# Performance work log

Measured on AMD Instinct MI355X. Metric: run time of the kernel, lower is better.

Reference implementation:

```python
import jax, jax.numpy as jnp
import numpy as np
import math

D_MODEL = 1024
N_HEAD = 16
B, T = 4, 2048


def setup_inputs() -> dict:
    key = jax.random.key(0)
    ks = jax.random.split(key, 12)
    s = 1.0 / math.sqrt(D_MODEL)
    inp = {
        "q": jax.random.normal(ks[0], (B, T, D_MODEL), dtype=jnp.float32),
        "k": jax.random.normal(ks[1], (B, T, D_MODEL), dtype=jnp.float32),
        "v": jax.random.normal(ks[2], (B, T, D_MODEL), dtype=jnp.float32),
        "Wq": jax.random.uniform(ks[3], (D_MODEL, D_MODEL), jnp.float32, -s, s),
        "bq": jax.random.uniform(ks[4], (D_MODEL,), jnp.float32, -s, s),
        "Wk": jax.random.uniform(ks[5], (D_MODEL, D_MODEL), jnp.float32, -s, s),
        "bk": jax.random.uniform(ks[6], (D_MODEL,), jnp.float32, -s, s),
        "Wv": jax.random.uniform(ks[7], (D_MODEL, D_MODEL), jnp.float32, -s, s),
        "bv": jax.random.uniform(ks[8], (D_MODEL,), jnp.float32, -s, s),
        "Wo": jax.random.uniform(ks[9], (D_MODEL, D_MODEL), jnp.float32, -s, s),
        "bo": jax.random.uniform(ks[10], (D_MODEL,), jnp.float32, -s, s),
    }
    return inp


def reference(q, k, v, Wq, bq, Wk, bk, Wv, bv, Wo, bo):
    # NOTE: original module applies all three projections to `q` (k, v args unused)
    batch, time, dim = q.shape
    n_d = dim // N_HEAD
    # torch Linear: x @ W.T + b
    Q = (q @ Wq.T + bq).reshape(batch, time, N_HEAD, n_d).transpose(0, 2, 1, 3)
    K = (q @ Wk.T + bk).reshape(batch, time, N_HEAD, n_d).transpose(0, 2, 1, 3)
    V = (q @ Wv.T + bv).reshape(batch, time, N_HEAD, n_d).transpose(0, 2, 1, 3)
    # [B, H, T, T]
    score = jnp.einsum("bhqd,bhkd->bhqk", Q, K) / jnp.sqrt(jnp.float32(n_d))
    causal = jnp.tril(jnp.ones((time, time), dtype=bool))
    score = jnp.where(causal, score, -jnp.inf)
    # original uses Softmax(dim=-2): normalizes over the QUERY axis (faithful)
    attn = jax.nn.softmax(score, axis=-2)
    ctx = jnp.einsum("bhqk,bhkd->bhqd", attn, V)
    ctx = ctx.transpose(0, 2, 1, 3).reshape(batch, time, dim)
    return ctx @ Wo.T + bo
```

## Files before the change

kernel.cpp:

```cpp
#include <hip/hip_runtime.h>
#include <hip/hip_bf16.h>
#include <cstdint>
#include <cstddef>

typedef __bf16 bf16x8 __attribute__((ext_vector_type(8)));
typedef __bf16 bf16x4 __attribute__((ext_vector_type(4)));
typedef __bf16 bf16x2 __attribute__((ext_vector_type(2)));
typedef float  f32x4  __attribute__((ext_vector_type(4)));

static constexpr int TSEQ  = 2048;
static constexpr int DM    = 1024;
static constexpr int NH    = 16;
static constexpr int HD    = 64;
static constexpr int BATCH = 4;
static constexpr float SCL = 0.18033688011112042f;

__device__ __forceinline__ void gload16(const __bf16* g, __bf16* l) {
  __builtin_amdgcn_global_load_lds((const __attribute__((address_space(1))) void*)g,
                                   (__attribute__((address_space(3))) void*)l, 16, 0, 0);
}

#define PBAR()  asm volatile("s_barrier" ::: "memory")
#define LGKM0() do { asm volatile("s_waitcnt lgkmcnt(0)" ::: "memory"); \
                     __builtin_amdgcn_sched_barrier(0); } while (0)

__global__ __launch_bounds__(256) void cvt_kernel(const float* __restrict__ in,
                                                  __bf16* __restrict__ out, int n4) {
  int i = blockIdx.x * 256 + threadIdx.x;
  if (i < n4) {
    float4 v = reinterpret_cast<const float4*>(in)[i];
    bf16x4 o;
    o[0] = (__bf16)v.x; o[1] = (__bf16)v.y; o[2] = (__bf16)v.z; o[3] = (__bf16)v.w;
    reinterpret_cast<bf16x4*>(out)[i] = o;
  }
}

__global__ __launch_bounds__(256) void cvt4_kernel(
    const float* __restrict__ a, const float* __restrict__ bsrc,
    const float* __restrict__ c, const float* __restrict__ d,
    __bf16* __restrict__ oa, __bf16* __restrict__ ob,
    __bf16* __restrict__ oc, __bf16* __restrict__ od, int n4) {
  const float* src = (blockIdx.y == 0) ? a : (blockIdx.y == 1) ? bsrc
                    : (blockIdx.y == 2) ? c : d;
  __bf16* dst = (blockIdx.y == 0) ? oa : (blockIdx.y == 1) ? ob
               : (blockIdx.y == 2) ? oc : od;
  int i = blockIdx.x * 256 + threadIdx.x;
  if (i < n4) {
    float4 v = reinterpret_cast<const float4*>(src)[i];
    bf16x4 o;
    o[0] = (__bf16)v.x; o[1] = (__bf16)v.y; o[2] = (__bf16)v.z; o[3] = (__bf16)v.w;
    reinterpret_cast<bf16x4*>(dst)[i] = o;
  }
}

template <typename OUT_T>
__device__ __forceinline__ void gemm_body8(
    const __bf16* __restrict__ A, const __bf16* __restrict__ W,
    const float* __restrict__ bias, OUT_T* __restrict__ C,
    int i0, int o0, __bf16* lA, __bf16* lB) {
  const int tid = threadIdx.x;
  const int l = tid & 63, lr = l & 15, lg = l >> 4;
  const int w = tid >> 6;
  const int wr = w >> 2, wc = w & 3;

  f32x4 acc[8][4];
  const f32x4 fzero = {0.f, 0.f, 0.f, 0.f};
#pragma unroll
  for (int mi = 0; mi < 8; ++mi)
#pragma unroll
    for (int ni = 0; ni < 4; ++ni) acc[mi][ni] = fzero;

  const int s_row = tid >> 3;
  const int s_cc  = tid & 7;
  const __bf16* Ab = A + (size_t)i0 * DM;
  const __bf16* Wb = W + (size_t)o0 * DM;

  auto stage = [&](const __bf16* G, __bf16* L, int buf, int kt, int h) {
#pragma unroll
    for (int rr = 0; rr < 2; ++rr) {
      int row = h * 128 + rr * 64 + s_row;
      gload16(G + (size_t)row * DM + kt * 64 + ((s_cc ^ (row & 7)) << 3),
              L + buf * 16384 + (h * 128 + rr * 64) * 64 + tid * 8);
    }
  };
  auto rd = [&](const __bf16* base, int row, int ks) {
    int chunk = (ks * 4 + lg) ^ (row & 7);
    return *(const bf16x8*)(base + row * 64 + chunk * 8);
  };

  const int NT = DM / 64;

#pragma unroll
  for (int h = 0; h < 2; ++h) { stage(Ab, lA, 0, 0, h); stage(Wb, lB, 0, 0, h); }
#pragma unroll
  for (int h = 0; h < 2; ++h) { stage(Ab, lA, 1, 1, h); stage(Wb, lB, 1, 1, h); }
  asm volatile("s_waitcnt vmcnt(8)" ::: "memory");
  PBAR();

  for (int t = 0; t < NT; ++t) {
    const int cur = t & 1;
    const __bf16* cA = lA + cur * 16384;
    const __bf16* cB = lB + cur * 16384;
    const bool pre = (t + 2 < NT);

    bf16x8 afl[4][2], bfl[2][2], afh[4][2], bfh[2][2];

#pragma unroll
    for (int mi = 0; mi < 4; ++mi)
#pragma unroll
      for (int ks = 0; ks < 2; ++ks)
        afl[mi][ks] = rd(cA, wr * 64 + mi * 16 + lr, ks);
#pragma unroll
    for (int ni = 0; ni < 2; ++ni)
#pragma unroll
      for (int ks = 0; ks < 2; ++ks)
        bfl[ni][ks] = rd(cB, wc * 32 + ni * 16 + lr, ks);
    PBAR(); LGKM0();
    __builtin_amdgcn_s_setprio(1);
#pragma unroll
    for (int mi = 0; mi < 4; ++mi)
#pragma unroll
      for (int ni = 0; ni < 2; ++ni)
#pragma unroll
        for (int ks = 0; ks < 2; ++ks)
          acc[mi][ni] = __builtin_amdgcn_mfma_f32_16x16x32_bf16(
              afl[mi][ks], bfl[ni][ks], acc[mi][ni], 0, 0, 0);
    __builtin_amdgcn_s_setprio(0);
    PBAR();

#pragma unroll
    for (int ni = 0; ni < 2; ++ni)
#pragma unroll
      for (int ks = 0; ks < 2; ++ks)
        bfh[ni][ks] = rd(cB, 128 + wc * 32 + ni * 16 + lr, ks);
    if (pre) stage(Wb, lB, cur, t + 2, 0);
    PBAR(); LGKM0();
    __builtin_amdgcn_s_setprio(1);
#pragma unroll
    for (int mi = 0; mi < 4; ++mi)
#pragma unroll
      for (int ni = 0; ni < 2; ++ni)
#pragma unroll
        for (int ks = 0; ks < 2; ++ks)
          acc[mi][ni + 2] = __builtin_amdgcn_mfma_f32_16x16x32_bf16(
              afl[mi][ks], bfh[ni][ks], acc[mi][ni + 2], 0, 0, 0);
    __builtin_amdgcn_s_setprio(0);
    PBAR();

#pragma unroll
    for (int mi = 0; mi < 4; ++mi)
#pragma unroll
      for (int ks = 0; ks < 2; ++ks)
        afh[mi][ks] = rd(cA, 128 + wr * 64 + mi * 16 + lr, ks);
    if (pre) { stage(Ab, lA, cur, t + 2, 0); stage(Wb, lB, cur, t + 2, 1); }
    PBAR(); LGKM0();
    __builtin_amdgcn_s_setprio(1);
#pragma unroll
    for (int mi = 0; mi < 4; ++mi)
#pragma unroll
      for (int ni = 0; ni < 2; ++ni)
#pragma unroll
        for (int ks = 0; ks < 2; ++ks)
          acc[mi + 4][ni] = __builtin_amdgcn_mfma_f32_16x16x32_bf16(
              afh[mi][ks], bfl[ni][ks], acc[mi + 4][ni], 0, 0, 0);
    __builtin_amdgcn_s_setprio(0);
    PBAR();

    if (pre) stage(Ab, lA, cur, t + 2, 1);
    if (pre)                asm volatile("s_waitcnt vmcnt(8)" ::: "memory");
    else if (t + 1 < NT)    asm volatile("s_waitcnt vmcnt(0)" ::: "memory");
    PBAR();
    __builtin_amdgcn_s_setprio(1);
#pragma unroll
    for (int mi = 0; mi < 4; ++mi)
#pragma unroll
      for (int ni = 0; ni < 2; ++ni)
#pragma unroll
        for (int ks = 0; ks < 2; ++ks)
          acc[mi + 4][ni + 2] = __builtin_amdgcn_mfma_f32_16x16x32_bf16(
              afh[mi][ks], bfh[ni][ks], acc[mi + 4][ni + 2], 0, 0, 0);
    __builtin_amdgcn_s_setprio(0);
    PBAR();
  }

#pragma unroll
  for (int ni = 0; ni < 4; ++ni) {
    int colb = (ni < 2) ? (wc * 32 + ni * 16) : (128 + wc * 32 + (ni - 2) * 16);
    int col = o0 + colb + lr;
    float bb = bias[col];
#pragma unroll
    for (int mi = 0; mi < 8; ++mi) {
      int rowb = (mi < 4) ? (wr * 64 + mi * 16) : (128 + wr * 64 + (mi - 4) * 16);
      int row = i0 + rowb + lg * 4;
#pragma unroll
      for (int r = 0; r < 4; ++r)
        C[(size_t)(row + r) * DM + col] = (OUT_T)(acc[mi][ni][r] + bb);
    }
  }
}

__global__ __launch_bounds__(512, 2) void gemm_qkv_kernel(
    const __bf16* __restrict__ A,
    const __bf16* __restrict__ W0, const __bf16* __restrict__ W1,
    const __bf16* __restrict__ W2,
    const float* __restrict__ b0, const float* __restrict__ b1,
    const float* __restrict__ b2,
    __bf16* __restrict__ O0, __bf16* __restrict__ O1, __bf16* __restrict__ O2) {
  __shared__ __align__(16) __bf16 lA[2 * 256 * 64];
  __shared__ __align__(16) __bf16 lB[2 * 256 * 64];
  const int flat = blockIdx.x;
  const int xcd = flat & 7, idx = flat >> 3;
  const int mi = xcd * 4 + idx / 12;
  const int nig = idx % 12;
  const int z = nig >> 2;
  const int o0 = (nig & 3) * 256;
  const __bf16* W = (z == 0) ? W0 : (z == 1) ? W1 : W2;
  const float* bias = (z == 0) ? b0 : (z == 1) ? b1 : b2;
  __bf16* C = (z == 0) ? O0 : (z == 1) ? O1 : O2;
  gemm_body8<__bf16>(A, W, bias, C, mi * 256, o0, lA, lB);
}

template <typename OUT_T>
__device__ __forceinline__ void gemm_body2(
    const __bf16* __restrict__ A, const __bf16* __restrict__ W,
    const float* __restrict__ bias, OUT_T* __restrict__ C,
    int i0, int o0, __bf16* lA, __bf16* lB) {
  const int tid = threadIdx.x;
  const int l = tid & 63, lr = l & 15, lg = l >> 4;
  const int w = tid >> 6;
  const int wr = w >> 2, wc = w & 3;

  f32x4 acc[4][4];
  const f32x4 fzero = {0.f, 0.f, 0.f, 0.f};
#pragma unroll
  for (int mi = 0; mi < 4; ++mi)
#pragma unroll
    for (int ni = 0; ni < 4; ++ni) acc[mi][ni] = fzero;

  const int s_row = tid >> 3;
  const int s_cc  = tid & 7;
  const int NT = DM / 64;

  {
#pragma unroll
    for (int n = 0; n < 2; ++n) {
      int row = n * 64 + s_row;
      gload16(A + (size_t)(i0 + row) * DM + ((s_cc ^ (row & 7)) << 3),
              lA + n * 4096 + tid * 8);
    }
#pragma unroll
    for (int n = 0; n < 4; ++n) {
      int row = n * 64 + s_row;
      gload16(W + (size_t)(o0 + row) * DM + ((s_cc ^ (row & 7)) << 3),
              lB + n * 4096 + tid * 8);
    }
  }
  asm volatile("s_waitcnt vmcnt(0)" ::: "memory");
  __syncthreads();

  for (int t = 0; t < NT; ++t) {
    const int cur = t & 1;
    if (t + 1 < NT) {
      const int k0 = (t + 1) * 64;
      const int nxt = cur ^ 1;
#pragma unroll
      for (int n = 0; n < 2; ++n) {
        int row = n * 64 + s_row;
        gload16(A + (size_t)(i0 + row) * DM + k0 + ((s_cc ^ (row & 7)) << 3),
                lA + nxt * 8192 + n * 4096 + tid * 8);
      }
#pragma unroll
      for (int n = 0; n < 4; ++n) {
        int row = n * 64 + s_row;
        gload16(W + (size_t)(o0 + row) * DM + k0 + ((s_cc ^ (row & 7)) << 3),
                lB + nxt * 16384 + n * 4096 + tid * 8);
      }
    }

    const __bf16* cA = lA + cur * 8192;
    const __bf16* cB = lB + cur * 16384;

    bf16x8 af[4][2], bf_[2][2];
#pragma unroll
    for (int mi = 0; mi < 4; ++mi)
#pragma unroll
      for (int ks = 0; ks < 2; ++ks) {
        int row = wr * 64 + mi * 16 + lr;
        int chunk = (ks * 4 + lg) ^ (row & 7);
        af[mi][ks] = *(const bf16x8*)(cA + row * 64 + chunk * 8);
      }
#pragma unroll
    for (int ni = 0; ni < 2; ++ni)
#pragma unroll
      for (int ks = 0; ks < 2; ++ks) {
        int row = wc * 64 + ni * 16 + lr;
        int chunk = (ks * 4 + lg) ^ (row & 7);
        bf_[ni][ks] = *(const bf16x8*)(cB + row * 64 + chunk * 8);
      }
    __builtin_amdgcn_s_setprio(1);
#pragma unroll
    for (int mi = 0; mi < 4; ++mi)
#pragma unroll
      for (int ni = 0; ni < 2; ++ni)
#pragma unroll
        for (int ks = 0; ks < 2; ++ks)
          acc[mi][ni] = __builtin_amdgcn_mfma_f32_16x16x32_bf16(
              af[mi][ks], bf_[ni][ks], acc[mi][ni], 0, 0, 0);
    __builtin_amdgcn_s_setprio(0);

#pragma unroll
    for (int ni = 0; ni < 2; ++ni)
#pragma unroll
      for (int ks = 0; ks < 2; ++ks) {
        int row = wc * 64 + (ni + 2) * 16 + lr;
        int chunk = (ks * 4 + lg) ^ (row & 7);
        bf_[ni][ks] = *(const bf16x8*)(cB + row * 64 + chunk * 8);
      }
    __builtin_amdgcn_s_setprio(1);
#pragma unroll
    for (int mi = 0; mi < 4; ++mi)
#pragma unroll
      for (int ni = 0; ni < 2; ++ni)
#pragma unroll
        for (int ks = 0; ks < 2; ++ks)
          acc[mi][ni + 2] = __builtin_amdgcn_mfma_f32_16x16x32_bf16(
              af[mi][ks], bf_[ni][ks], acc[mi][ni + 2], 0, 0, 0);
    __builtin_amdgcn_s_setprio(0);

    if (t + 1 < NT) {
      asm volatile("s_waitcnt vmcnt(0)" ::: "memory");
      __syncthreads();
    }
  }

#pragma unroll
  for (int ni = 0; ni < 4; ++ni) {
    int col = o0 + wc * 64 + ni * 16 + lr;
    float bb = bias[col];
#pragma unroll
    for (int mi = 0; mi < 4; ++mi) {
      int row = i0 + wr * 64 + mi * 16 + lg * 4;
#pragma unroll
      for (int r = 0; r < 4; ++r)
        C[(size_t)(row + r) * DM + col] = (OUT_T)(acc[mi][ni][r] + bb);
    }
  }
}

__global__ __launch_bounds__(512, 2) void gemm_out_kernel(
    const __bf16* __restrict__ A, const __bf16* __restrict__ W,
    const float* __restrict__ bias, float* __restrict__ C) {
  __shared__ __align__(16) __bf16 lA[2 * 128 * 64];
  __shared__ __align__(16) __bf16 lB[2 * 256 * 64];
  const int flat = blockIdx.x;
  const int xcd = flat & 7, idx = flat >> 3;
  const int mi = xcd * 8 + (idx & 7);
  const int ni = idx >> 3;
  gemm_body2<float>(A, W, bias, C, mi * 128, ni * 256, lA, lB);
}

__global__ __launch_bounds__(256) void colstats_kernel(
    const __bf16* __restrict__ Q, const __bf16* __restrict__ K,
    const __bf16* __restrict__ V, __bf16* __restrict__ VT) {
  const int flat = blockIdx.x;
  const int wid = (flat & 7) * 128 + (flat >> 3);
  const int g = wid >> 4, bx = wid & 15;
  const int h = g & 15, b = g >> 4;
  const int tid = threadIdx.x;
  const int w = tid >> 6, l = tid & 63, lr = l & 15, lg = l >> 4;
  const size_t base = (size_t)b * TSEQ * DM + (size_t)h * HD;

  __shared__ float part[4][64];
  __shared__ float invc[64];

  for (int ph = 0; ph < 2; ++ph) {
    const int kt = ph ? (31 - bx) : bx;
    const int k0 = kt * 64;

    bf16x8 kf[4][2];
#pragma unroll
    for (int ct = 0; ct < 4; ++ct)
#pragma unroll
      for (int ks = 0; ks < 2; ++ks)
        kf[ct][ks] = *(const bf16x8*)(K + base + (size_t)(k0 + ct * 16 + lr) * DM +
                                      ks * 32 + lg * 8);

    float csum[4] = {0.f, 0.f, 0.f, 0.f};
    const int nchunks = (TSEQ - k0) >> 4;
    for (int jj = w; jj < nchunks; jj += 4) {
      int qrow = k0 + jj * 16;
      bf16x8 a0 = *(const bf16x8*)(Q + base + (size_t)(qrow + lr) * DM + lg * 8);
      bf16x8 a1 = *(const bf16x8*)(Q + base + (size_t)(qrow + lr) * DM + 32 + lg * 8);
      const bool interior = (jj >= 4);
#pragma unroll
      for (int ct = 0; ct < 4; ++ct) {
        f32x4 s = {0.f, 0.f, 0.f, 0.f};
        s = __builtin_amdgcn_mfma_f32_16x16x32_bf16(a0, kf[ct][0], s, 0, 0, 0);
        s = __builtin_amdgcn_mfma_f32_16x16x32_bf16(a1, kf[ct][1], s, 0, 0, 0);
        if (interior) {
#pragma unroll
          for (int r = 0; r < 4; ++r) csum[ct] += __builtin_amdgcn_exp2f(s[r] * SCL);
        } else {
#pragma unroll
          for (int r = 0; r < 4; ++r) {
            int ql = jj * 16 + lg * 4 + r;
            int kl = ct * 16 + lr;
            float e = __builtin_amdgcn_exp2f(s[r] * SCL);
            csum[ct] += (ql >= kl) ? e : 0.f;
          }
        }
      }
    }

#pragma unroll
    for (int ct = 0; ct < 4; ++ct) {
      csum[ct] += __shfl_xor(csum[ct], 16, 64);
      csum[ct] += __shfl_xor(csum[ct], 32, 64);
    }

    if (l < 16) {
#pragma unroll
      for (int ct = 0; ct < 4; ++ct) part[w][ct * 16 + l] = csum[ct];
    }
    __syncthreads();
    if (tid < 64) {
      float c = part[0][tid] + part[1][tid] + part[2][tid] + part[3][tid];
      invc[tid] = 1.0f / c;
    }
    __syncthreads();

    const int d = tid >> 2, gq = tid & 3;
    size_t vtb = (((size_t)(b * NH + h)) * HD + d) * TSEQ + k0 + gq * 16;
#pragma unroll
    for (int kc = 0; kc < 16; kc += 2) {
      int kl = gq * 16 + kc;
      float v0 = (float)V[base + (size_t)(k0 + kl) * DM + d] * invc[kl];
      float v1 = (float)V[base + (size_t)(k0 + kl + 1) * DM + d] * invc[kl + 1];
      bf16x2 o; o[0] = (__bf16)v0; o[1] = (__bf16)v1;
      *(bf16x2*)(VT + vtb + kc) = o;
    }
    __syncthreads();
  }
}

__device__ __forceinline__ int swz(int e) { return e ^ (((e >> 6) & 7) << 3); }

__global__ __launch_bounds__(256) void ctx_kernel(
    const __bf16* __restrict__ Q, const __bf16* __restrict__ K,
    const __bf16* __restrict__ VT, __bf16* __restrict__ CTX) {
  __shared__ __align__(16) __bf16 lK[4096];
  __shared__ __align__(16) __bf16 lV[4096];
  __shared__ __align__(16) __bf16 lP[4][16 * 88];
  const int flat = blockIdx.x;
  const int wid = (flat & 7) * 128 + (flat >> 3);
  const int g = wid >> 4, bx = wid & 15;
  const int h = g & 15, b = g >> 4;
  const int tid = threadIdx.x;
  const int w = tid >> 6, l = tid & 63, lr = l & 15, lg = l >> 4;
  const size_t base = (size_t)b * TSEQ * DM + (size_t)h * HD;
  const size_t vtb = ((size_t)(b * NH + h)) * HD * TSEQ;
  __bf16* pw = &lP[w][0];

  const int srow = w * 8 + (l >> 3);
  const int scol = (((l & 7) ^ (l >> 3)) << 3);

  for (int ph = 0; ph < 2; ++ph) {
    const int qt = ph ? bx : 31 - bx;
    const int q0 = qt * 64;

    bf16x8 qf[2];
#pragma unroll
    for (int ks = 0; ks < 2; ++ks)
      qf[ks] = *(const bf16x8*)(Q + base + (size_t)(q0 + w * 16 + lr) * DM + ks * 32 + lg * 8);

    f32x4 acc[4];
    const f32x4 fzero = {0.f, 0.f, 0.f, 0.f};
#pragma unroll
    for (int dt = 0; dt < 4; ++dt) acc[dt] = fzero;

    for (int kt = 0; kt <= qt; ++kt) {
      const int k0 = kt * 64;
#pragma unroll
      for (int n = 0; n < 2; ++n) {
        gload16(K + base + (size_t)(k0 + n * 32 + srow) * DM + scol,
                lK + n * 2048 + w * 512);
        gload16(VT + vtb + (size_t)(n * 32 + srow) * TSEQ + k0 + scol,
                lV + n * 2048 + w * 512);
      }
      asm volatile("s_waitcnt vmcnt(0)" ::: "memory");
      __syncthreads();

      const bool diag = (kt == qt);
#pragma unroll
      for (int ct = 0; ct < 4; ++ct) {
        f32x4 s = {0.f, 0.f, 0.f, 0.f};
#pragma unroll
        for (int ks = 0; ks < 2; ++ks) {
          int e = (ct * 16 + lr) * 64 + ks * 32 + lg * 8;
          bf16x8 kb8 = *(const bf16x8*)(lK + swz(e));
          s = __builtin_amdgcn_mfma_f32_16x16x32_bf16(kb8, qf[ks], s, 0, 0, 0);
        }
        bf16x4 pk;
        if (diag) {
#pragma unroll
          for (int r = 0; r < 4; ++r) {
            int ql = w * 16 + lr;
            int kl = ct * 16 + lg * 4 + r;
            float pv = (ql >= kl) ? __builtin_amdgcn_exp2f(s[r] * SCL) : 0.f;
            pk[r] = (__bf16)pv;
          }
        } else {
#pragma unroll
          for (int r = 0; r < 4; ++r)
            pk[r] = (__bf16)__builtin_amdgcn_exp2f(s[r] * SCL);
        }
        *(bf16x4*)(pw + lr * 88 + ct * 16 + lg * 4) = pk;
      }
      asm volatile("" ::: "memory");

      bf16x8 pa[2];
#pragma unroll
      for (int ks = 0; ks < 2; ++ks)
        pa[ks] = *(const bf16x8*)(pw + lr * 88 + ks * 32 + lg * 8);
#pragma unroll
      for (int dt = 0; dt < 4; ++dt) {
#pragma unroll
        for (int ks = 0; ks < 2; ++ks) {
          int e = (dt * 16 + lr) * 64 + ks * 32 + lg * 8;
          bf16x8 vb8 = *(const bf16x8*)(lV + swz(e));
          acc[dt] = __builtin_amdgcn_mfma_f32_16x16x32_bf16(pa[ks], vb8, acc[dt], 0, 0, 0);
        }
      }
      __syncthreads();
    }

#pragma unroll
    for (int dt = 0; dt < 4; ++dt)
#pragma unroll
      for (int r = 0; r < 4; ++r)
        CTX[base + (size_t)(q0 + w * 16 + lg * 4 + r) * DM + dt * 16 + lr] = (__bf16)acc[dt][r];
  }
}

extern "C" void kernel_launch(void* const* d_in, const int* in_sizes, int n_in,
                              void* d_out, int out_size, void* d_ws, size_t ws_size,
                              hipStream_t stream) {
  const float* q  = (const float*)d_in[0];
  const float* Wq = (const float*)d_in[3];
  const float* bq = (const float*)d_in[4];
  const float* Wk = (const float*)d_in[5];
  const float* bk = (const float*)d_in[6];
  const float* Wv = (const float*)d_in[7];
  const float* bv = (const float*)d_in[8];
  const float* Wo = (const float*)d_in[9];
  const float* bo = (const float*)d_in[10];
  float* out = (float*)d_out;

  const size_t NTOK = (size_t)BATCH * TSEQ;
  char* ws = (char*)d_ws;
  __bf16* qb  = (__bf16*)ws; ws += NTOK * DM * 2;
  __bf16* Wqb = (__bf16*)ws; ws += (size_t)DM * DM * 2;
  __bf16* Wkb = (__bf16*)ws; ws += (size_t)DM * DM * 2;
  __bf16* Wvb = (__bf16*)ws; ws += (size_t)DM * DM * 2;
  __bf16* Wob = (__bf16*)ws; ws += (size_t)DM * DM * 2;
  __bf16* Qp  = (__bf16*)ws; ws += NTOK * DM * 2;
  __bf16* Kp  = (__bf16*)ws; ws += NTOK * DM * 2;
  __bf16* Vp  = (__bf16*)ws; ws += NTOK * DM * 2;
  __bf16* VT  = (__bf16*)ws; ws += (size_t)BATCH * NH * HD * TSEQ * 2;
  __bf16* CTX = qb;

  const int nq4 = (int)(NTOK * DM / 4);
  const int nw4 = DM * DM / 4;
  cvt_kernel<<<(nq4 + 255) / 256, 256, 0, stream>>>(q, qb, nq4);
  cvt4_kernel<<<dim3((nw4 + 255) / 256, 4), 256, 0, stream>>>(
      Wq, Wk, Wv, Wo, Wqb, Wkb, Wvb, Wob, nw4);

  gemm_qkv_kernel<<<384, 512, 0, stream>>>(qb, Wqb, Wkb, Wvb, bq, bk, bv,
                                           Qp, Kp, Vp);

  colstats_kernel<<<1024, 256, 0, stream>>>(Qp, Kp, Vp, VT);
  ctx_kernel<<<1024, 256, 0, stream>>>(Qp, Kp, VT, CTX);

  gemm_out_kernel<<<256, 512, 0, stream>>>(CTX, Wob, bo, out);
}
```

Baseline: 218.9 us.

## Double-buffer K/V tiles in ctx kernel and drop GEMM sched barriers

The attention context kernel now keeps two LDS buffers for K and V and issues the global-to-LDS loads for the next key tile before computing on the current one, so load latency overlaps with the MFMA work. This costs an extra 16 KB of LDS per block, which may lower occupancy. The GEMM kernel also drops the sched_barrier after its lgkmcnt waits, letting the compiler schedule instructions across those points more freely.

```diff
diff --git a/kernel.cpp b/kernel.cpp
--- a/kernel.cpp
+++ b/kernel.cpp
@@ -21,8 +21,7 @@
 }
 
 #define PBAR()  asm volatile("s_barrier" ::: "memory")
-#define LGKM0() do { asm volatile("s_waitcnt lgkmcnt(0)" ::: "memory"); \
-                     __builtin_amdgcn_sched_barrier(0); } while (0)
+#define LGKM()  asm volatile("s_waitcnt lgkmcnt(0)" ::: "memory")
 
 __global__ __launch_bounds__(256) void cvt_kernel(const float* __restrict__ in,
                                                   __bf16* __restrict__ out, int n4) {
@@ -115,7 +114,7 @@
 #pragma unroll
       for (int ks = 0; ks < 2; ++ks)
         bfl[ni][ks] = rd(cB, wc * 32 + ni * 16 + lr, ks);
-    PBAR(); LGKM0();
+    PBAR(); LGKM();
     __builtin_amdgcn_s_setprio(1);
 #pragma unroll
     for (int mi = 0; mi < 4; ++mi)
@@ -134,7 +133,7 @@
       for (int ks = 0; ks < 2; ++ks)
         bfh[ni][ks] = rd(cB, 128 + wc * 32 + ni * 16 + lr, ks);
     if (pre) stage(Wb, lB, cur, t + 2, 0);
-    PBAR(); LGKM0();
+    PBAR(); LGKM();
     __builtin_amdgcn_s_setprio(1);
 #pragma unroll
     for (int mi = 0; mi < 4; ++mi)
@@ -153,7 +152,7 @@
       for (int ks = 0; ks < 2; ++ks)
         afh[mi][ks] = rd(cA, 128 + wr * 64 + mi * 16 + lr, ks);
     if (pre) { stage(Ab, lA, cur, t + 2, 0); stage(Wb, lB, cur, t + 2, 1); }
-    PBAR(); LGKM0();
+    PBAR(); LGKM();
     __builtin_amdgcn_s_setprio(1);
 #pragma unroll
     for (int mi = 0; mi < 4; ++mi)
@@ -448,8 +447,8 @@
 __global__ __launch_bounds__(256) void ctx_kernel(
     const __bf16* __restrict__ Q, const __bf16* __restrict__ K,
     const __bf16* __restrict__ VT, __bf16* __restrict__ CTX) {
-  __shared__ __align__(16) __bf16 lK[4096];
-  __shared__ __align__(16) __bf16 lV[4096];
+  __shared__ __align__(16) __bf16 lK[2][4096];
+  __shared__ __align__(16) __bf16 lV[2][4096];
   __shared__ __align__(16) __bf16 lP[4][16 * 88];
   const int flat = blockIdx.x;
   const int wid = (flat & 7) * 128 + (flat >> 3);
@@ -464,6 +463,17 @@
   const int srow = w * 8 + (l >> 3);
   const int scol = (((l & 7) ^ (l >> 3)) << 3);
 
+  auto stageKV = [&](int kt, int buf) {
+    const int k0 = kt * 64;
+#pragma unroll
+    for (int n = 0; n < 2; ++n) {
+      gload16(K + base + (size_t)(k0 + n * 32 + srow) * DM + scol,
+              &lK[buf][0] + n * 2048 + w * 512);
+      gload16(VT + vtb + (size_t)(n * 32 + srow) * TSEQ + k0 + scol,
+              &lV[buf][0] + n * 2048 + w * 512);
+    }
+  };
+
   for (int ph = 0; ph < 2; ++ph) {
     const int qt = ph ? bx : 31 - bx;
     const int q0 = qt * 64;
@@ -478,18 +488,17 @@
 #pragma unroll
     for (int dt = 0; dt < 4; ++dt) acc[dt] = fzero;
 
+    __syncthreads();
+    stageKV(0, 0);
+    asm volatile("s_waitcnt vmcnt(0)" ::: "memory");
+    __syncthreads();
+
     for (int kt = 0; kt <= qt; ++kt) {
-      const int k0 = kt * 64;
-#pragma unroll
-      for (int n = 0; n < 2; ++n) {
-        gload16(K + base + (size_t)(k0 + n * 32 + srow) * DM + scol,
-                lK + n * 2048 + w * 512);
-        gload16(VT + vtb + (size_t)(n * 32 + srow) * TSEQ + k0 + scol,
-                lV + n * 2048 + w * 512);
-      }
-      asm volatile("s_waitcnt vmcnt(0)" ::: "memory");
-      __syncthreads();
-
+      const int cur = kt & 1;
+      if (kt < qt) stageKV(kt + 1, cur ^ 1);
+
+      const __bf16* cK = &lK[cur][0];
+      const __bf16* cV = &lV[cur][0];
       const bool diag = (kt == qt);
 #pragma unroll
       for (int ct = 0; ct < 4; ++ct) {
@@ -497,7 +506,7 @@
 #pragma unroll
         for (int ks = 0; ks < 2; ++ks) {
           int e = (ct * 16 + lr) * 64 + ks * 32 + lg * 8;
-          bf16x8 kb8 = *(const bf16x8*)(lK + swz(e));
+          bf16x8 kb8 = *(const bf16x8*)(cK + swz(e));
           s = __builtin_amdgcn_mfma_f32_16x16x32_bf16(kb8, qf[ks], s, 0, 0, 0);
         }
         bf16x4 pk;
@@ -527,11 +536,15 @@
 #pragma unroll
         for (int ks = 0; ks < 2; ++ks) {
           int e = (dt * 16 + lr) * 64 + ks * 32 + lg * 8;
-          bf16x8 vb8 = *(const bf16x8*)(lV + swz(e));
+          bf16x8 vb8 = *(const bf16x8*)(cV + swz(e));
           acc[dt] = __builtin_amdgcn_mfma_f32_16x16x32_bf16(pa[ks], vb8, acc[dt], 0, 0, 0);
         }
       }
-      __syncthreads();
+
+      if (kt < qt) {
+        asm volatile("s_waitcnt vmcnt(0)" ::: "memory");
+        __syncthreads();
+      }
     }
 
 #pragma unroll
```

After: 228.4 us. 4.3% more time.

## Share K/V tile loads across both query tiles in ctx kernel

Applied to the files above, without the earlier changes.

The ctx kernel used to process its two query tiles (31-bx and bx) one after the other, loading the K and V^T tiles for each separately. It now runs a single key loop in which each loaded K/V tile feeds both query tiles while the second is still active. This roughly halves global-to-LDS traffic for the shorter tile, at the cost of more registers and LDS for a second P buffer. The change also adds a launch-bounds occupancy hint and removes sched_barrier from the GEMM's lgkmcnt wait macro, giving the compiler more freedom to schedule.

```diff
diff --git a/kernel.cpp b/kernel.cpp
--- a/kernel.cpp
+++ b/kernel.cpp
@@ -21,8 +21,7 @@
 }
 
 #define PBAR()  asm volatile("s_barrier" ::: "memory")
-#define LGKM0() do { asm volatile("s_waitcnt lgkmcnt(0)" ::: "memory"); \
-                     __builtin_amdgcn_sched_barrier(0); } while (0)
+#define LGKM()  asm volatile("s_waitcnt lgkmcnt(0)" ::: "memory")
 
 __global__ __launch_bounds__(256) void cvt_kernel(const float* __restrict__ in,
                                                   __bf16* __restrict__ out, int n4) {
@@ -115,7 +114,7 @@
 #pragma unroll
       for (int ks = 0; ks < 2; ++ks)
         bfl[ni][ks] = rd(cB, wc * 32 + ni * 16 + lr, ks);
-    PBAR(); LGKM0();
+    PBAR(); LGKM();
     __builtin_amdgcn_s_setprio(1);
 #pragma unroll
     for (int mi = 0; mi < 4; ++mi)
@@ -134,7 +133,7 @@
       for (int ks = 0; ks < 2; ++ks)
         bfh[ni][ks] = rd(cB, 128 + wc * 32 + ni * 16 + lr, ks);
     if (pre) stage(Wb, lB, cur, t + 2, 0);
-    PBAR(); LGKM0();
+    PBAR(); LGKM();
     __builtin_amdgcn_s_setprio(1);
 #pragma unroll
     for (int mi = 0; mi < 4; ++mi)
@@ -153,7 +152,7 @@
       for (int ks = 0; ks < 2; ++ks)
         afh[mi][ks] = rd(cA, 128 + wr * 64 + mi * 16 + lr, ks);
     if (pre) { stage(Ab, lA, cur, t + 2, 0); stage(Wb, lB, cur, t + 2, 1); }
-    PBAR(); LGKM0();
+    PBAR(); LGKM();
     __builtin_amdgcn_s_setprio(1);
 #pragma unroll
     for (int mi = 0; mi < 4; ++mi)
@@ -445,12 +444,12 @@
 
 __device__ __forceinline__ int swz(int e) { return e ^ (((e >> 6) & 7) << 3); }
 
-__global__ __launch_bounds__(256) void ctx_kernel(
+__global__ __launch_bounds__(256, 4) void ctx_kernel(
     const __bf16* __restrict__ Q, const __bf16* __restrict__ K,
     const __bf16* __restrict__ VT, __bf16* __restrict__ CTX) {
   __shared__ __align__(16) __bf16 lK[4096];
   __shared__ __align__(16) __bf16 lV[4096];
-  __shared__ __align__(16) __bf16 lP[4][16 * 88];
+  __shared__ __align__(16) __bf16 lP[8][16 * 88];
   const int flat = blockIdx.x;
   const int wid = (flat & 7) * 128 + (flat >> 3);
   const int g = wid >> 4, bx = wid & 15;
@@ -459,87 +458,118 @@
   const int w = tid >> 6, l = tid & 63, lr = l & 15, lg = l >> 4;
   const size_t base = (size_t)b * TSEQ * DM + (size_t)h * HD;
   const size_t vtb = ((size_t)(b * NH + h)) * HD * TSEQ;
-  __bf16* pw = &lP[w][0];
+  __bf16* pw1 = &lP[w][0];
+  __bf16* pw2 = &lP[w + 4][0];
+
+  const int qt1 = 31 - bx, qt2 = bx;
+  const int q01 = qt1 * 64, q02 = qt2 * 64;
 
   const int srow = w * 8 + (l >> 3);
   const int scol = (((l & 7) ^ (l >> 3)) << 3);
 
-  for (int ph = 0; ph < 2; ++ph) {
-    const int qt = ph ? bx : 31 - bx;
-    const int q0 = qt * 64;
-
-    bf16x8 qf[2];
-#pragma unroll
-    for (int ks = 0; ks < 2; ++ks)
-      qf[ks] = *(const bf16x8*)(Q + base + (size_t)(q0 + w * 16 + lr) * DM + ks * 32 + lg * 8);
-
-    f32x4 acc[4];
-    const f32x4 fzero = {0.f, 0.f, 0.f, 0.f};
-#pragma unroll
-    for (int dt = 0; dt < 4; ++dt) acc[dt] = fzero;
-
-    for (int kt = 0; kt <= qt; ++kt) {
-      const int k0 = kt * 64;
-#pragma unroll
-      for (int n = 0; n < 2; ++n) {
-        gload16(K + base + (size_t)(k0 + n * 32 + srow) * DM + scol,
-                lK + n * 2048 + w * 512);
-        gload16(VT + vtb + (size_t)(n * 32 + srow) * TSEQ + k0 + scol,
-                lV + n * 2048 + w * 512);
-      }
-      asm volatile("s_waitcnt vmcnt(0)" ::: "memory");
-      __syncthreads();
-
-      const bool diag = (kt == qt);
-#pragma unroll
-      for (int ct = 0; ct < 4; ++ct) {
+  bf16x8 qf1[2], qf2[2];
+#pragma unroll
+  for (int ks = 0; ks < 2; ++ks) {
+    qf1[ks] = *(const bf16x8*)(Q + base + (size_t)(q01 + w * 16 + lr) * DM + ks * 32 + lg * 8);
+    qf2[ks] = *(const bf16x8*)(Q + base + (size_t)(q02 + w * 16 + lr) * DM + ks * 32 + lg * 8);
+  }
+
+  f32x4 acc1[4], acc2[4];
+  const f32x4 fzero = {0.f, 0.f, 0.f, 0.f};
+#pragma unroll
+  for (int dt = 0; dt < 4; ++dt) { acc1[dt] = fzero; acc2[dt] = fzero; }
+
+  for (int kt = 0; kt <= qt1; ++kt) {
+    const int k0 = kt * 64;
+    const bool two = (kt <= qt2);
+    __syncthreads();
+#pragma unroll
+    for (int n = 0; n < 2; ++n) {
+      gload16(K + base + (size_t)(k0 + n * 32 + srow) * DM + scol,
+              lK + n * 2048 + w * 512);
+      gload16(VT + vtb + (size_t)(n * 32 + srow) * TSEQ + k0 + scol,
+              lV + n * 2048 + w * 512);
+    }
+    asm volatile("s_waitcnt vmcnt(0)" ::: "memory");
+    __syncthreads();
+
+    const bool diag1 = (kt == qt1), diag2 = (kt == qt2);
+#pragma unroll
+    for (int ct = 0; ct < 4; ++ct) {
+      bf16x8 kb[2];
+#pragma unroll
+      for (int ks = 0; ks < 2; ++ks) {
+        int e = (ct * 16 + lr) * 64 + ks * 32 + lg * 8;
+        kb[ks] = *(const bf16x8*)(lK + swz(e));
+      }
+      {
         f32x4 s = {0.f, 0.f, 0.f, 0.f};
-#pragma unroll
-        for (int ks = 0; ks < 2; ++ks) {
-          int e = (ct * 16 + lr) * 64 + ks * 32 + lg * 8;
-          bf16x8 kb8 = *(const bf16x8*)(lK + swz(e));
-          s = __builtin_amdgcn_mfma_f32_16x16x32_bf16(kb8, qf[ks], s, 0, 0, 0);
-        }
+        s = __builtin_amdgcn_mfma_f32_16x16x32_bf16(kb[0], qf1[0], s, 0, 0, 0);
+        s = __builtin_amdgcn_mfma_f32_16x16x32_bf16(kb[1], qf1[1], s, 0, 0, 0);
         bf16x4 pk;
-        if (diag) {
+        if (diag1) {
 #pragma unroll
           for (int r = 0; r < 4; ++r) {
-            int ql = w * 16 + lr;
-            int kl = ct * 16 + lg * 4 + r;
-            float pv = (ql >= kl) ? __builtin_amdgcn_exp2f(s[r] * SCL) : 0.f;
-            pk[r] = (__bf16)pv;
+            int ql = w * 16 + lr, kl = ct * 16 + lg * 4 + r;
+            pk[r] = (__bf16)((ql >= kl) ? __builtin_amdgcn_exp2f(s[r] * SCL) : 0.f);
           }
         } else {
 #pragma unroll
           for (int r = 0; r < 4; ++r)
             pk[r] = (__bf16)__builtin_amdgcn_exp2f(s[r] * SCL);
         }
-        *(bf16x4*)(pw + lr * 88 + ct * 16 + lg * 4) = pk;
-      }
-      asm volatile("" ::: "memory");
-
-      bf16x8 pa[2];
+        *(bf16x4*)(pw1 + lr * 88 + ct * 16 + lg * 4) = pk;
+      }
+      if (two) {
+        f32x4 s = {0.f, 0.f, 0.f, 0.f};
+        s = __builtin_amdgcn_mfma_f32_16x16x32_bf16(kb[0], qf2[0], s, 0, 0, 0);
+        s = __builtin_amdgcn_mfma_f32_16x16x32_bf16(kb[1], qf2[1], s, 0, 0, 0);
+        bf16x4 pk;
+        if (diag2) {
+#pragma unroll
+          for (int r = 0; r < 4; ++r) {
+            int ql = w * 16 + lr, kl = ct * 16 + lg * 4 + r;
+            pk[r] = (__bf16)((ql >= kl) ? __builtin_amdgcn_exp2f(s[r] * SCL) : 0.f);
+          }
+        } else {
+#pragma unroll
+          for (int r = 0; r < 4; ++r)
+            pk[r] = (__bf16)__builtin_amdgcn_exp2f(s[r] * SCL);
+        }
+        *(bf16x4*)(pw2 + lr * 88 + ct * 16 + lg * 4) = pk;
+      }
+    }
+    asm volatile("" ::: "memory");
+
+    bf16x8 pa1[2], pa2[2];
+#pragma unroll
+    for (int ks = 0; ks < 2; ++ks)
+      pa1[ks] = *(const bf16x8*)(pw1 + lr * 88 + ks * 32 + lg * 8);
+    if (two) {
 #pragma unroll
       for (int ks = 0; ks < 2; ++ks)
-        pa[ks] = *(const bf16x8*)(pw + lr * 88 + ks * 32 + lg * 8);
-#pragma unroll
-      for (int dt = 0; dt < 4; ++dt) {
-#pragma unroll
-        for (int ks = 0; ks < 2; ++ks) {
-          int e = (dt * 16 + lr) * 64 + ks * 32 + lg * 8;
-          bf16x8 vb8 = *(const bf16x8*)(lV + swz(e));
-          acc[dt] = __builtin_amdgcn_mfma_f32_16x16x32_bf16(pa[ks], vb8, acc[dt], 0, 0, 0);
-        }
-      }
-      __syncthreads();
-    }
-
-#pragma unroll
-    for (int dt = 0; dt < 4; ++dt)
-#pragma unroll
-      for (int r = 0; r < 4; ++r)
-        CTX[base + (size_t)(q0 + w * 16 + lg * 4 + r) * DM + dt * 16 + lr] = (__bf16)acc[dt][r];
-  }
+        pa2[ks] = *(const bf16x8*)(pw2 + lr * 88 + ks * 32 + lg * 8);
+    }
+#pragma unroll
+    for (int dt = 0; dt < 4; ++dt) {
+#pragma unroll
+      for (int ks = 0; ks < 2; ++ks) {
+        int e = (dt * 16 + lr) * 64 + ks * 32 + lg * 8;
+        bf16x8 vb8 = *(const bf16x8*)(lV + swz(e));
+        acc1[dt] = __builtin_amdgcn_mfma_f32_16x16x32_bf16(pa1[ks], vb8, acc1[dt], 0, 0, 0);
+        if (two)
+          acc2[dt] = __builtin_amdgcn_mfma_f32_16x16x32_bf16(pa2[ks], vb8, acc2[dt], 0, 0, 0);
+      }
+    }
+  }
+
+#pragma unroll
+  for (int dt = 0; dt < 4; ++dt)
+#pragma unroll
+    for (int r = 0; r < 4; ++r) {
+      CTX[base + (size_t)(q01 + w * 16 + lg * 4 + r) * DM + dt * 16 + lr] = (__bf16)acc1[dt][r];
+      CTX[base + (size_t)(q02 + w * 16 + lg * 4 + r) * DM + dt * 16 + lr] = (__bf16)acc2[dt][r];
+    }
 }
 
 extern "C" void kernel_launch(void* const* d_in, const int* in_sizes, int n_in,
```

Result: faster. 208.7 us (-4.7%).

## Process four query tiles per ctx block to reuse K/V tile loads

Applied to the files above, without the earlier changes.

The ctx kernel now handles four query tiles per block (balanced pairs 31-bx, 23-bx, 8+bx, bx) instead of two sequential phases. Each K/V tile loaded into LDS is reused across all active query tiles, which cuts global K/V traffic and barriers per unit of work, and the grid is halved. The cost is more registers for four accumulator sets (launch bounds set to 2 blocks per SM) and more LDS for per-tile P buffers. The GEMM wait macro also drops its sched_barrier, giving the compiler freedom to reorder around the lgkmcnt wait.

```diff
diff --git a/kernel.cpp b/kernel.cpp
--- a/kernel.cpp
+++ b/kernel.cpp
@@ -21,8 +21,7 @@
 }
 
 #define PBAR()  asm volatile("s_barrier" ::: "memory")
-#define LGKM0() do { asm volatile("s_waitcnt lgkmcnt(0)" ::: "memory"); \
-                     __builtin_amdgcn_sched_barrier(0); } while (0)
+#define LGKM()  asm volatile("s_waitcnt lgkmcnt(0)" ::: "memory")
 
 __global__ __launch_bounds__(256) void cvt_kernel(const float* __restrict__ in,
                                                   __bf16* __restrict__ out, int n4) {
@@ -115,7 +114,7 @@
 #pragma unroll
       for (int ks = 0; ks < 2; ++ks)
         bfl[ni][ks] = rd(cB, wc * 32 + ni * 16 + lr, ks);
-    PBAR(); LGKM0();
+    PBAR(); LGKM();
     __builtin_amdgcn_s_setprio(1);
 #pragma unroll
     for (int mi = 0; mi < 4; ++mi)
@@ -134,7 +133,7 @@
       for (int ks = 0; ks < 2; ++ks)
         bfh[ni][ks] = rd(cB, 128 + wc * 32 + ni * 16 + lr, ks);
     if (pre) stage(Wb, lB, cur, t + 2, 0);
-    PBAR(); LGKM0();
+    PBAR(); LGKM();
     __builtin_amdgcn_s_setprio(1);
 #pragma unroll
     for (int mi = 0; mi < 4; ++mi)
@@ -153,7 +152,7 @@
       for (int ks = 0; ks < 2; ++ks)
         afh[mi][ks] = rd(cA, 128 + wr * 64 + mi * 16 + lr, ks);
     if (pre) { stage(Ab, lA, cur, t + 2, 0); stage(Wb, lB, cur, t + 2, 1); }
-    PBAR(); LGKM0();
+    PBAR(); LGKM();
     __builtin_amdgcn_s_setprio(1);
 #pragma unroll
     for (int mi = 0; mi < 4; ++mi)
@@ -445,101 +444,117 @@
 
 __device__ __forceinline__ int swz(int e) { return e ^ (((e >> 6) & 7) << 3); }
 
-__global__ __launch_bounds__(256) void ctx_kernel(
+__global__ __launch_bounds__(256, 2) void ctx_kernel(
     const __bf16* __restrict__ Q, const __bf16* __restrict__ K,
     const __bf16* __restrict__ VT, __bf16* __restrict__ CTX) {
   __shared__ __align__(16) __bf16 lK[4096];
   __shared__ __align__(16) __bf16 lV[4096];
-  __shared__ __align__(16) __bf16 lP[4][16 * 88];
+  __shared__ __align__(16) __bf16 lP[4][4][16 * 88];
   const int flat = blockIdx.x;
-  const int wid = (flat & 7) * 128 + (flat >> 3);
-  const int g = wid >> 4, bx = wid & 15;
+  const int wid = (flat & 7) * 64 + (flat >> 3);
+  const int g = wid >> 3, bx = wid & 7;
   const int h = g & 15, b = g >> 4;
   const int tid = threadIdx.x;
   const int w = tid >> 6, l = tid & 63, lr = l & 15, lg = l >> 4;
   const size_t base = (size_t)b * TSEQ * DM + (size_t)h * HD;
   const size_t vtb = ((size_t)(b * NH + h)) * HD * TSEQ;
-  __bf16* pw = &lP[w][0];
+
+  const int qt[4] = {31 - bx, 23 - bx, 8 + bx, bx};
 
   const int srow = w * 8 + (l >> 3);
   const int scol = (((l & 7) ^ (l >> 3)) << 3);
 
-  for (int ph = 0; ph < 2; ++ph) {
-    const int qt = ph ? bx : 31 - bx;
-    const int q0 = qt * 64;
-
-    bf16x8 qf[2];
+  bf16x8 qf[4][2];
+#pragma unroll
+  for (int i = 0; i < 4; ++i)
 #pragma unroll
     for (int ks = 0; ks < 2; ++ks)
-      qf[ks] = *(const bf16x8*)(Q + base + (size_t)(q0 + w * 16 + lr) * DM + ks * 32 + lg * 8);
-
-    f32x4 acc[4];
-    const f32x4 fzero = {0.f, 0.f, 0.f, 0.f};
-#pragma unroll
-    for (int dt = 0; dt < 4; ++dt) acc[dt] = fzero;
-
-    for (int kt = 0; kt <= qt; ++kt) {
-      const int k0 = kt * 64;
-#pragma unroll
-      for (int n = 0; n < 2; ++n) {
-        gload16(K + base + (size_t)(k0 + n * 32 + srow) * DM + scol,
-                lK + n * 2048 + w * 512);
-        gload16(VT + vtb + (size_t)(n * 32 + srow) * TSEQ + k0 + scol,
-                lV + n * 2048 + w * 512);
-      }
-      asm volatile("s_waitcnt vmcnt(0)" ::: "memory");
-      __syncthreads();
-
-      const bool diag = (kt == qt);
-#pragma unroll
-      for (int ct = 0; ct < 4; ++ct) {
-        f32x4 s = {0.f, 0.f, 0.f, 0.f};
-#pragma unroll
-        for (int ks = 0; ks < 2; ++ks) {
-          int e = (ct * 16 + lr) * 64 + ks * 32 + lg * 8;
-          bf16x8 kb8 = *(const bf16x8*)(lK + swz(e));
-          s = __builtin_amdgcn_mfma_f32_16x16x32_bf16(kb8, qf[ks], s, 0, 0, 0);
+      qf[i][ks] = *(const bf16x8*)(Q + base +
+          (size_t)(qt[i] * 64 + w * 16 + lr) * DM + ks * 32 + lg * 8);
+
+  f32x4 acc[4][4];
+  const f32x4 fzero = {0.f, 0.f, 0.f, 0.f};
+#pragma unroll
+  for (int i = 0; i < 4; ++i)
+#pragma unroll
+    for (int dt = 0; dt < 4; ++dt) acc[i][dt] = fzero;
+
+  for (int kt = 0; kt <= qt[0]; ++kt) {
+    const int k0 = kt * 64;
+    __syncthreads();
+#pragma unroll
+    for (int n = 0; n < 2; ++n) {
+      gload16(K + base + (size_t)(k0 + n * 32 + srow) * DM + scol,
+              lK + n * 2048 + w * 512);
+      gload16(VT + vtb + (size_t)(n * 32 + srow) * TSEQ + k0 + scol,
+              lV + n * 2048 + w * 512);
+    }
+    asm volatile("s_waitcnt vmcnt(0)" ::: "memory");
+    __syncthreads();
+
+#pragma unroll
+    for (int ct = 0; ct < 4; ++ct) {
+      bf16x8 kb[2];
+#pragma unroll
+      for (int ks = 0; ks < 2; ++ks) {
+        int e = (ct * 16 + lr) * 64 + ks * 32 + lg * 8;
+        kb[ks] = *(const bf16x8*)(lK + swz(e));
+      }
+#pragma unroll
+      for (int i = 0; i < 4; ++i) {
+        if (kt <= qt[i]) {
+          f32x4 s = {0.f, 0.f, 0.f, 0.f};
+          s = __builtin_amdgcn_mfma_f32_16x16x32_bf16(kb[0], qf[i][0], s, 0, 0, 0);
+          s = __builtin_amdgcn_mfma_f32_16x16x32_bf16(kb[1], qf[i][1], s, 0, 0, 0);
+          bf16x4 pk;
+          if (kt == qt[i]) {
+#pragma unroll
+            for (int r = 0; r < 4; ++r) {
+              int ql = w * 16 + lr, kl = ct * 16 + lg * 4 + r;
+              pk[r] = (__bf16)((ql >= kl) ? __builtin_amdgcn_exp2f(s[r] * SCL) : 0.f);
+            }
+          } else {
+#pragma unroll
+            for (int r = 0; r < 4; ++r)
+              pk[r] = (__bf16)__builtin_amdgcn_exp2f(s[r] * SCL);
+          }
+          *(bf16x4*)(&lP[w][i][lr * 88 + ct * 16 + lg * 4]) = pk;
         }
-        bf16x4 pk;
-        if (diag) {
-#pragma unroll
-          for (int r = 0; r < 4; ++r) {
-            int ql = w * 16 + lr;
-            int kl = ct * 16 + lg * 4 + r;
-            float pv = (ql >= kl) ? __builtin_amdgcn_exp2f(s[r] * SCL) : 0.f;
-            pk[r] = (__bf16)pv;
-          }
-        } else {
-#pragma unroll
-          for (int r = 0; r < 4; ++r)
-            pk[r] = (__bf16)__builtin_amdgcn_exp2f(s[r] * SCL);
-        }
-        *(bf16x4*)(pw + lr * 88 + ct * 16 + lg * 4) = pk;
-      }
-      asm volatile("" ::: "memory");
-
-      bf16x8 pa[2];
-#pragma unroll
-      for (int ks = 0; ks < 2; ++ks)
-        pa[ks] = *(const bf16x8*)(pw + lr * 88 + ks * 32 + lg * 8);
-#pragma unroll
-      for (int dt = 0; dt < 4; ++dt) {
-#pragma unroll
-        for (int ks = 0; ks < 2; ++ks) {
-          int e = (dt * 16 + lr) * 64 + ks * 32 + lg * 8;
-          bf16x8 vb8 = *(const bf16x8*)(lV + swz(e));
-          acc[dt] = __builtin_amdgcn_mfma_f32_16x16x32_bf16(pa[ks], vb8, acc[dt], 0, 0, 0);
-        }
-      }
-      __syncthreads();
-    }
-
+      }
+    }
+    asm volatile("" ::: "memory");
+
+    bf16x8 pa[4][2];
+#pragma unroll
+    for (int i = 0; i < 4; ++i)
+      if (kt <= qt[i]) {
+#pragma unroll
+        for (int ks = 0; ks < 2; ++ks)
+          pa[i][ks] = *(const bf16x8*)(&lP[w][i][lr * 88 + ks * 32 + lg * 8]);
+      }
+#pragma unroll
+    for (int dt = 0; dt < 4; ++dt) {
+#pragma unroll
+      for (int ks = 0; ks < 2; ++ks) {
+        int e = (dt * 16 + lr) * 64 + ks * 32 + lg * 8;
+        bf16x8 vb8 = *(const bf16x8*)(lV + swz(e));
+#pragma unroll
+        for (int i = 0; i < 4; ++i)
+          if (kt <= qt[i])
+            acc[i][dt] = __builtin_amdgcn_mfma_f32_16x16x32_bf16(
+                pa[i][ks], vb8, acc[i][dt], 0, 0, 0);
+      }
+    }
+  }
+
+#pragma unroll
+  for (int i = 0; i < 4; ++i)
 #pragma unroll
     for (int dt = 0; dt < 4; ++dt)
 #pragma unroll
       for (int r = 0; r < 4; ++r)
-        CTX[base + (size_t)(q0 + w * 16 + lg * 4 + r) * DM + dt * 16 + lr] = (__bf16)acc[dt][r];
-  }
+        CTX[base + (size_t)(qt[i] * 64 + w * 16 + lg * 4 + r) * DM + dt * 16 + lr] =
+            (__bf16)acc[i][dt][r];
 }
 
 extern "C" void kernel_launch(void* const* d_in, const int* in_sizes, int n_in,
@@ -579,7 +594,7 @@
                                            Qp, Kp, Vp);
 
   colstats_kernel<<<1024, 256, 0, stream>>>(Qp, Kp, Vp, VT);
-  ctx_kernel<<<1024, 256, 0, stream>>>(Qp, Kp, VT, CTX);
+  ctx_kernel<<<512, 256, 0, stream>>>(Qp, Kp, VT, CTX);
 
   gemm_out_kernel<<<256, 512, 0, stream>>>(CTX, Wob, bo, out);
 }
```

Measured after the change: 222.9 us. About the same (+1.8%).
